# Optimization experiments

Hardware: AMD Instinct MI355X
Metric: run time of the kernel (lower is better)

Reference implementation:

```python
import jax, jax.numpy as jnp
import numpy as np

N_NODES = 100000
N_EDGES = 1600000
NFEAT = 128
NHID = 128
NS = 64
NCLASS = 16
B = 8192


def setup_inputs() -> dict:
    key = jax.random.key(0)
    ks = jax.random.split(key, 12)
    s = jax.random.normal(ks[0], (B, NS), dtype=jnp.float32)
    x = jax.random.normal(ks[1], (N_NODES, NFEAT), dtype=jnp.float32)
    row = jax.random.randint(ks[2], (N_EDGES,), 0, N_NODES)
    col = jax.random.randint(ks[3], (N_EDGES,), 0, N_NODES)
    val = jax.random.uniform(ks[4], (N_EDGES,), dtype=jnp.float32)
    index = jax.random.randint(ks[5], (B,), 0, N_NODES)
    # learned parameters (glorot-ish scale)
    W1 = jax.random.normal(ks[6], (NFEAT, NHID), dtype=jnp.float32) / np.sqrt(NFEAT)
    b1 = jnp.zeros((NHID,), dtype=jnp.float32)
    W2 = jax.random.normal(ks[7], (NHID, NHID), dtype=jnp.float32) / np.sqrt(NHID)
    b2 = jnp.zeros((NHID,), dtype=jnp.float32)
    Wl = jax.random.normal(ks[8], (NHID + NS, NCLASS), dtype=jnp.float32) / np.sqrt(NHID + NS)
    bl = jnp.zeros((NCLASS,), dtype=jnp.float32)
    return {"s": s, "x": x, "row": row, "col": col, "val": val,
            "index": index, "W1": W1, "b1": b1, "W2": W2, "b2": b2,
            "Wl": Wl, "bl": bl}


def reference(s, x, row, col, val, index, W1, b1, W2, b2, Wl, bl):
    n = x.shape[0]

    def spmm(h):
        # adj @ h with adj in COO form: out[r] += val_e * h[c]
        return jax.ops.segment_sum(val[:, None] * h[col], row, num_segments=n)

    # dropout is identity in eval mode (training=False)
    h = jax.nn.relu(spmm(x @ W1) + b1)          # gc1 + relu
    h = spmm(h @ W2) + b2                        # gc2
    z = jnp.concatenate([h[index], s], axis=1) @ Wl + bl  # [B, nclass]
    return jax.nn.log_softmax(z, axis=1)
```

## Files before the change

kernel.cpp:

```cpp
#include <hip/hip_runtime.h>
#include <math.h>

#define N_NODES 100000
#define N_EDGES 1600000
#define NFEAT 128
#define NHID 128
#define NS 64
#define NCLASS 16
#define BB 8192

#define B1_SHIFT 11
#define NB1 49
#define SUB_SHIFT 5
#define NSUB 3125
#define CHUNKA 2048
#define HWG 256
#define BINC_CAP 2048

typedef unsigned long long ull;
typedef unsigned int uint;


__device__ __forceinline__ unsigned short f2bf(float f) {
  unsigned int u = __float_as_uint(f);
  return (unsigned short)((u + 0x7fffu + ((u >> 16) & 1u)) >> 16);
}
__device__ __forceinline__ float bflo(unsigned int u) {
  return __uint_as_float(u << 16);
}
__device__ __forceinline__ float bfhi(unsigned int u) {
  return __uint_as_float(u & 0xffff0000u);
}
__device__ __forceinline__ unsigned int packbf2(float lo, float hi) {
  return (unsigned int)f2bf(lo) | ((unsigned int)f2bf(hi) << 16);
}


__device__ __forceinline__ ull pack_edge(float v, int r, int c) {
  return ((ull)(__float_as_uint(v) >> 2) << 34) | ((ull)(unsigned)r << 17) | (unsigned)c;
}
__device__ __forceinline__ int edge_col(ull p) { return (int)(p & 0x1FFFFu); }
__device__ __forceinline__ int edge_row(ull p) { return (int)((unsigned)(p >> 17) & 0x1FFFFu); }
__device__ __forceinline__ float edge_val(ull p) {
  return __uint_as_float(((unsigned)(p >> 34)) << 2);
}
__device__ __forceinline__ int keep_test(const uint* keep, int r) {
  return (keep[r >> 5] >> (r & 31)) & 1u;
}


__global__ __launch_bounds__(256) void selbuild_kernel(const int* __restrict__ index,
                                                       int* __restrict__ sel,
                                                       uint* __restrict__ keep) {
  int t = blockIdx.x * 256 + threadIdx.x;
  int r = index[t];
  sel[r] = 1;
  atomicOr(&keep[r >> 5], 1u << (r & 31));
}

__global__ __launch_bounds__(256) void selflag_kernel(const int* __restrict__ row,
                                                      const int* __restrict__ col,
                                                      const int* __restrict__ sel,
                                                      uint* __restrict__ keep) {
  int i = blockIdx.x * blockDim.x + threadIdx.x;
  int stride = gridDim.x * blockDim.x;
  for (; i < N_EDGES; i += stride)
    if (sel[row[i]]) {
      int c = col[i];
      atomicOr(&keep[c >> 5], 1u << (c & 31));
    }
}


__global__ __launch_bounds__(256) void histsub_kernel(const int* __restrict__ row,
                                                      const uint* __restrict__ keep,
                                                      int* __restrict__ subcnt) {
  __shared__ int lh[NSUB];
  int tid = threadIdx.x;
  for (int i = tid; i < NSUB; i += 256) lh[i] = 0;
  __syncthreads();
  for (long i = (long)blockIdx.x * 256 + tid; i < N_EDGES; i += (long)HWG * 256) {
    int r = row[i];
    if (keep_test(keep, r)) atomicAdd(&lh[r >> SUB_SHIFT], 1);
  }
  __syncthreads();
  for (int i = tid; i < NSUB; i += 256) {
    int c = lh[i];
    if (c) atomicAdd(&subcnt[i], c);
  }
}


__global__ __launch_bounds__(1024) void scanall_kernel(const int* __restrict__ subcnt,
                                                       int* __restrict__ sub_offs,
                                                       int* __restrict__ gcur1,
                                                       int* __restrict__ gcur2) {
  __shared__ int sd[1024];
  int tid = threadIdx.x;
  int b0 = tid * 4;
  int vv[4];
  int loc = 0;
#pragma unroll
  for (int k = 0; k < 4; ++k) {
    int i = b0 + k;
    vv[k] = (i < NSUB) ? subcnt[i] : 0;
    loc += vv[k];
  }
  sd[tid] = loc;
  __syncthreads();
  for (int o = 1; o < 1024; o <<= 1) {
    int add = (tid >= o) ? sd[tid - o] : 0;
    __syncthreads();
    sd[tid] += add;
    __syncthreads();
  }
  int pre = sd[tid] - loc;
#pragma unroll
  for (int k = 0; k < 4; ++k) {
    int i = b0 + k;
    if (i < NSUB) {
      sub_offs[i] = pre;
      gcur2[i] = pre;
      if ((i & 63) == 0) gcur1[i >> 6] = pre;
      pre += vv[k];
    }
  }
  if (tid == 1023) sub_offs[NSUB] = sd[1023];
}


__global__ __launch_bounds__(256) void binA_kernel(const int* __restrict__ row,
                                                   const int* __restrict__ col,
                                                   const float* __restrict__ val,
                                                   const uint* __restrict__ keep,
                                                   int* __restrict__ gcur1,
                                                   ull* __restrict__ ebuf1) {
  __shared__ ull stage[CHUNKA];
  __shared__ short bkt[CHUNKA];
  __shared__ int hist[NB1], lofs[NB1 + 1], lcur[NB1], gbase[NB1];
  int tid = threadIdx.x;
  for (long base = (long)blockIdx.x * CHUNKA; base < N_EDGES; base += (long)gridDim.x * CHUNKA) {
    int cnt = (int)min((long)CHUNKA, (long)N_EDGES - base);
    if (tid < NB1) hist[tid] = 0;
    __syncthreads();
    ull e[8]; int bk[8];
#pragma unroll
    for (int v = 0; v < 8; ++v) {
      int i = v * 256 + tid;
      bk[v] = -1;
      if (i < cnt) {
        long g = base + i;
        int r = row[g];
        if (keep_test(keep, r)) {
          e[v] = pack_edge(val[g], r, col[g]);
          bk[v] = r >> B1_SHIFT;
          atomicAdd(&hist[bk[v]], 1);
        }
      }
    }
    __syncthreads();
    if (tid < 64) {
      int h = (tid < NB1) ? hist[tid] : 0;
      int x = h;
      for (int o = 1; o < 64; o <<= 1) {
        int y = __shfl_up(x, o);
        if (tid >= o) x += y;
      }
      if (tid < NB1) { lofs[tid] = x - h; lcur[tid] = x - h; }
      if (tid == 63) lofs[NB1] = x;
    }
    __syncthreads();
#pragma unroll
    for (int v = 0; v < 8; ++v) {
      if (bk[v] >= 0) {
        int pos = atomicAdd(&lcur[bk[v]], 1);
        stage[pos] = e[v];
        bkt[pos] = (short)bk[v];
      }
    }
    __syncthreads();
    if (tid < NB1) {
      int h = hist[tid];
      if (h > 0) gbase[tid] = atomicAdd(&gcur1[tid], h);
    }
    __syncthreads();
    int tot = lofs[NB1];
    for (int s = tid; s < tot; s += 256) {
      int lo = bkt[s];
      ebuf1[gbase[lo] + (s - lofs[lo])] = stage[s];
    }
    __syncthreads();
  }
}


__global__ __launch_bounds__(256) void binB_kernel(const ull* __restrict__ ebuf1,
                                                   const int* __restrict__ sub_offs,
                                                   int* __restrict__ gcur2,
                                                   ull* __restrict__ edat) {
  __shared__ ull stage[CHUNKA];
  __shared__ short bkt[CHUNKA];
  __shared__ int hist[64], lofs[65], lcur[64], gbase[64];
  int tid = threadIdx.x;
  int b1 = blockIdx.x >> 3, w = blockIdx.x & 7;
  int rbeg = sub_offs[b1 << 6];
  int rend = sub_offs[min((b1 + 1) << 6, NSUB)];
  for (int base = rbeg + w * CHUNKA; base < rend; base += 8 * CHUNKA) {
    int cnt = min(CHUNKA, rend - base);
    if (tid < 64) hist[tid] = 0;
    __syncthreads();
    ull e[8]; int bk[8];
#pragma unroll
    for (int v = 0; v < 8; ++v) {
      int i = v * 256 + tid;
      bk[v] = -1;
      if (i < cnt) {
        e[v] = ebuf1[base + i];
        bk[v] = (edge_row(e[v]) >> SUB_SHIFT) - (b1 << 6);
        atomicAdd(&hist[bk[v]], 1);
      }
    }
    __syncthreads();
    if (tid < 64) {
      int h = hist[tid];
      int x = h;
      for (int o = 1; o < 64; o <<= 1) {
        int y = __shfl_up(x, o);
        if (tid >= o) x += y;
      }
      lofs[tid] = x - h;
      lcur[tid] = x - h;
      if (tid == 63) lofs[64] = x;
    }
    __syncthreads();
#pragma unroll
    for (int v = 0; v < 8; ++v) {
      if (bk[v] >= 0) {
        int pos = atomicAdd(&lcur[bk[v]], 1);
        stage[pos] = e[v];
        bkt[pos] = (short)bk[v];
      }
    }
    __syncthreads();
    if (tid < 64) {
      int h = hist[tid];
      if (h > 0) gbase[tid] = atomicAdd(&gcur2[(b1 << 6) + tid], h);
    }
    __syncthreads();
    for (int s = tid; s < cnt; s += 256) {
      int lo = bkt[s];
      edat[gbase[lo] + (s - lofs[lo])] = stage[s];
    }
    __syncthreads();
  }
}


__global__ __launch_bounds__(256) void binC_kernel(const int* __restrict__ sub_offs,
                                                   ull* __restrict__ edat,
                                                   ull* __restrict__ ebuf1,
                                                   int* __restrict__ offs) {
  __shared__ ull es[BINC_CAP];
  __shared__ int rcnt[32], rcur[32];
  int s = blockIdx.x, tid = threadIdx.x;
  int r0 = s << SUB_SHIFT;
  int beg = sub_offs[s], end = sub_offs[s + 1];
  int n = end - beg;
  if (tid < 32) rcnt[tid] = 0;
  __syncthreads();
  if (n <= BINC_CAP) {
    for (int i = tid; i < n; i += 256) {
      ull p = edat[beg + i];
      es[i] = p;
      atomicAdd(&rcnt[edge_row(p) & 31], 1);
    }
    __syncthreads();
    if (tid < 32) {
      int h = rcnt[tid];
      int x = h;
      for (int o = 1; o < 32; o <<= 1) {
        int y = __shfl_up(x, o, 32);
        if (tid >= o) x += y;
      }
      rcur[tid] = x - h;
      offs[r0 + tid] = beg + x - h;
      if (s == NSUB - 1 && tid == 31) offs[N_NODES] = end;
    }
    __syncthreads();
    for (int i = tid; i < n; i += 256) {
      ull p = es[i];
      int pos = atomicAdd(&rcur[edge_row(p) & 31], 1);
      edat[beg + pos] = p;
    }
  } else {
    for (int i = tid; i < n; i += 256) {
      ull p = edat[beg + i];
      ebuf1[beg + i] = p;
      atomicAdd(&rcnt[edge_row(p) & 31], 1);
    }
    __syncthreads();
    if (tid < 32) {
      int h = rcnt[tid];
      int x = h;
      for (int o = 1; o < 32; o <<= 1) {
        int y = __shfl_up(x, o, 32);
        if (tid >= o) x += y;
      }
      rcur[tid] = x - h;
      offs[r0 + tid] = beg + x - h;
      if (s == NSUB - 1 && tid == 31) offs[N_NODES] = end;
    }
    __syncthreads();
    for (int i = tid; i < n; i += 256) {
      ull p = ebuf1[beg + i];
      int pos = atomicAdd(&rcur[edge_row(p) & 31], 1);
      edat[beg + pos] = p;
    }
  }
}


typedef __attribute__((ext_vector_type(8))) __bf16 bf16x8;
typedef __attribute__((ext_vector_type(4))) float f32x4;
union FragU { uint4 u; bf16x8 b; };

#define LDSTR 68

__global__ __launch_bounds__(256) void gemm1_kernel(const float* __restrict__ A,
                                                    const float* __restrict__ W,
                                                    unsigned short* __restrict__ C,
                                                    int nrows) {
  __shared__ uint As_s[64 * LDSTR];
  __shared__ uint Wt_s[128 * LDSTR];
  int tid = threadIdx.x;
  int rbase = blockIdx.x * 64;

  {
    int n = tid & 127, hh = tid >> 7;
#pragma unroll
    for (int kk = 0; kk < 32; ++kk) {
      int kc = hh * 32 + kk;
      Wt_s[n * LDSTR + kc] = packbf2(W[(2 * kc) * 128 + n], W[(2 * kc + 1) * 128 + n]);
    }
  }
  {
    const float4* src = (const float4*)(A + (long)rbase * 128);
#pragma unroll
    for (int i = 0; i < 8; ++i) {
      int f = i * 256 + tid;
      int m = f >> 5;
      float4 v = (rbase + m < nrows) ? src[f] : make_float4(0.f, 0.f, 0.f, 0.f);
      int c = (f & 31) * 2;
      As_s[m * LDSTR + c]     = packbf2(v.x, v.y);
      As_s[m * LDSTR + c + 1] = packbf2(v.z, v.w);
    }
  }
  __syncthreads();

  int w = tid >> 6, lane = tid & 63;
  int quad = lane >> 4, lr = lane & 15;
  int n0 = w * 32;

  f32x4 acc[4][2];
#pragma unroll
  for (int mt = 0; mt < 4; ++mt)
#pragma unroll
    for (int nt = 0; nt < 2; ++nt) acc[mt][nt] = (f32x4){0.f, 0.f, 0.f, 0.f};

#pragma unroll
  for (int kk = 0; kk < 4; ++kk) {
    int kc = kk * 16 + quad * 4;
    FragU fb0, fb1;
    fb0.u = *(const uint4*)&Wt_s[(n0 + lr) * LDSTR + kc];
    fb1.u = *(const uint4*)&Wt_s[(n0 + 16 + lr) * LDSTR + kc];
#pragma unroll
    for (int mt = 0; mt < 4; ++mt) {
      FragU fa;
      fa.u = *(const uint4*)&As_s[(mt * 16 + lr) * LDSTR + kc];
      acc[mt][0] = __builtin_amdgcn_mfma_f32_16x16x32_bf16(fa.b, fb0.b, acc[mt][0], 0, 0, 0);
      acc[mt][1] = __builtin_amdgcn_mfma_f32_16x16x32_bf16(fa.b, fb1.b, acc[mt][1], 0, 0, 0);
    }
  }

#pragma unroll
  for (int mt = 0; mt < 4; ++mt) {
#pragma unroll
    for (int nt = 0; nt < 2; ++nt) {
      int col = n0 + nt * 16 + lr;
#pragma unroll
      for (int r = 0; r < 4; ++r) {
        int row = rbase + mt * 16 + quad * 4 + r;
        if (row < nrows) C[(long)row * 128 + col] = f2bf(acc[mt][nt][r]);
      }
    }
  }
}


__global__ __launch_bounds__(256) void gemm2f_kernel(const float* __restrict__ g2,
                                                     const float* __restrict__ W2,
                                                     const float* __restrict__ b2,
                                                     const float* __restrict__ s_in,
                                                     const float* __restrict__ Wl,
                                                     const float* __restrict__ bl,
                                                     float* __restrict__ out) {
  __shared__ uint smem[13056];
  uint* Wt_s = smem;
  uint* As_s = smem + 128 * LDSTR;
  float* ts  = (float*)smem;
  float* Wls = (float*)(smem + 128 * LDSTR);
  int tid = threadIdx.x;
  int rbase = blockIdx.x * 64;

  {
    int n = tid & 127, hh = tid >> 7;
#pragma unroll
    for (int kk = 0; kk < 32; ++kk) {
      int kc = hh * 32 + kk;
      Wt_s[n * LDSTR + kc] = packbf2(W2[(2 * kc) * 128 + n], W2[(2 * kc + 1) * 128 + n]);
    }
  }
  {
    const float4* src = (const float4*)(g2 + (long)rbase * 128);
#pragma unroll
    for (int i = 0; i < 8; ++i) {
      int f = i * 256 + tid;
      int m = f >> 5, c = (f & 31) * 2;
      float4 v = src[f];
      As_s[m * LDSTR + c]     = packbf2(v.x, v.y);
      As_s[m * LDSTR + c + 1] = packbf2(v.z, v.w);
    }
  }
  __syncthreads();

  int w = tid >> 6, lane = tid & 63;
  int quad = lane >> 4, lr = lane & 15;
  int n0 = w * 32;

  f32x4 acc[4][2];
#pragma unroll
  for (int mt = 0; mt < 4; ++mt)
#pragma unroll
    for (int nt = 0; nt < 2; ++nt) acc[mt][nt] = (f32x4){0.f, 0.f, 0.f, 0.f};

#pragma unroll
  for (int kk = 0; kk < 4; ++kk) {
    int kc = kk * 16 + quad * 4;
    FragU fb0, fb1;
    fb0.u = *(const uint4*)&Wt_s[(n0 + lr) * LDSTR + kc];
    fb1.u = *(const uint4*)&Wt_s[(n0 + 16 + lr) * LDSTR + kc];
#pragma unroll
    for (int mt = 0; mt < 4; ++mt) {
      FragU fa;
      fa.u = *(const uint4*)&As_s[(mt * 16 + lr) * LDSTR + kc];
      acc[mt][0] = __builtin_amdgcn_mfma_f32_16x16x32_bf16(fa.b, fb0.b, acc[mt][0], 0, 0, 0);
      acc[mt][1] = __builtin_amdgcn_mfma_f32_16x16x32_bf16(fa.b, fb1.b, acc[mt][1], 0, 0, 0);
    }
  }
  __syncthreads();

#pragma unroll
  for (int mt = 0; mt < 4; ++mt) {
#pragma unroll
    for (int nt = 0; nt < 2; ++nt) {
      int col = n0 + nt * 16 + lr;
      float bv = b2[col];
#pragma unroll
      for (int r = 0; r < 4; ++r)
        ts[(mt * 16 + quad * 4 + r) * 129 + col] = acc[mt][nt][r] + bv;
    }
  }
  for (int i = tid; i < 192 * 16; i += 256) Wls[i] = Wl[i];
  __syncthreads();

  int q = lane & 3;
  int mrow = w * 16 + (lane >> 2);
  int b = rbase + mrow;
  float z[16];
#pragma unroll
  for (int c = 0; c < 16; ++c) z[c] = 0.f;
  int k0 = q * 48;
  for (int kk = 0; kk < 48; ++kk) {
    int k = k0 + kk;
    float xv = (k < 128) ? ts[mrow * 129 + k] : s_in[(long)b * 64 + (k - 128)];
    const float* wp = Wls + k * 16;
#pragma unroll
    for (int c = 0; c < 16; ++c) z[c] = fmaf(xv, wp[c], z[c]);
  }
#pragma unroll
  for (int c = 0; c < 16; ++c) {
    z[c] += __shfl_xor(z[c], 1);
    z[c] += __shfl_xor(z[c], 2);
  }
  if (q == 0) {
#pragma unroll
    for (int c = 0; c < 16; ++c) z[c] += bl[c];
    float mx = z[0];
#pragma unroll
    for (int c = 1; c < 16; ++c) mx = fmaxf(mx, z[c]);
    float sum = 0.f;
#pragma unroll
    for (int c = 0; c < 16; ++c) sum += expf(z[c] - mx);
    float lse = mx + logf(sum);
    float4* ob = (float4*)(out + (long)b * 16);
    ob[0] = make_float4(z[0] - lse, z[1] - lse, z[2] - lse, z[3] - lse);
    ob[1] = make_float4(z[4] - lse, z[5] - lse, z[6] - lse, z[7] - lse);
    ob[2] = make_float4(z[8] - lse, z[9] - lse, z[10] - lse, z[11] - lse);
    ob[3] = make_float4(z[12] - lse, z[13] - lse, z[14] - lse, z[15] - lse);
  }
}


__device__ __forceinline__ void fma_row(float* acc, float v, uint4 u) {
  acc[0] = fmaf(v, bflo(u.x), acc[0]);
  acc[1] = fmaf(v, bfhi(u.x), acc[1]);
  acc[2] = fmaf(v, bflo(u.y), acc[2]);
  acc[3] = fmaf(v, bfhi(u.y), acc[3]);
  acc[4] = fmaf(v, bflo(u.z), acc[4]);
  acc[5] = fmaf(v, bfhi(u.z), acc[5]);
  acc[6] = fmaf(v, bflo(u.w), acc[6]);
  acc[7] = fmaf(v, bfhi(u.w), acc[7]);
}

__global__ __launch_bounds__(256) void spmm_row_kernel(const int* __restrict__ offs,
                                                       const ull* __restrict__ edat,
                                                       const unsigned short* __restrict__ a,
                                                       const float* __restrict__ bias,
                                                       unsigned short* __restrict__ h,
                                                       const uint* __restrict__ keep) {
  int wave = threadIdx.x >> 6;
  int lane = threadIdx.x & 63;
  int r = blockIdx.x * 4 + wave;
  if (!keep_test(keep, r)) return;
  int g = lane >> 4, l = lane & 15;
  int s = offs[r], e = offs[r + 1];
  float acc[8] = {0.f, 0.f, 0.f, 0.f, 0.f, 0.f, 0.f, 0.f};
  int j = s + g;
  for (; j + 4 < e; j += 8) {
    ull p0 = edat[j];
    ull p1 = edat[j + 4];
    uint4 u0 = *(const uint4*)(a + (long)edge_col(p0) * 128 + l * 8);
    uint4 u1 = *(const uint4*)(a + (long)edge_col(p1) * 128 + l * 8);
    fma_row(acc, edge_val(p0), u0);
    fma_row(acc, edge_val(p1), u1);
  }
  if (j < e) {
    ull p = edat[j];
    uint4 u = *(const uint4*)(a + (long)edge_col(p) * 128 + l * 8);
    fma_row(acc, edge_val(p), u);
  }
#pragma unroll
  for (int k = 0; k < 8; ++k) {
    acc[k] += __shfl_xor(acc[k], 16);
    acc[k] += __shfl_xor(acc[k], 32);
  }
  if (g == 0) {
    float4 b0 = *(const float4*)(bias + l * 8);
    float4 b1 = *(const float4*)(bias + l * 8 + 4);
    uint4 o;
    o.x = packbf2(fmaxf(acc[0] + b0.x, 0.f), fmaxf(acc[1] + b0.y, 0.f));
    o.y = packbf2(fmaxf(acc[2] + b0.z, 0.f), fmaxf(acc[3] + b0.w, 0.f));
    o.z = packbf2(fmaxf(acc[4] + b1.x, 0.f), fmaxf(acc[5] + b1.y, 0.f));
    o.w = packbf2(fmaxf(acc[6] + b1.z, 0.f), fmaxf(acc[7] + b1.w, 0.f));
    *(uint4*)(h + (long)r * 128 + l * 8) = o;
  }
}

__global__ __launch_bounds__(256) void spmm_sel_kernel(const int* __restrict__ offs,
                                                       const ull* __restrict__ edat,
                                                       const unsigned short* __restrict__ h1,
                                                       const int* __restrict__ index,
                                                       float* __restrict__ g2) {
  int wave = threadIdx.x >> 6;
  int lane = threadIdx.x & 63;
  int b = blockIdx.x * 4 + wave;
  int g = lane >> 4, l = lane & 15;
  int r = index[b];
  int s = offs[r], e = offs[r + 1];
  float acc[8] = {0.f, 0.f, 0.f, 0.f, 0.f, 0.f, 0.f, 0.f};
  int j = s + g;
  for (; j + 4 < e; j += 8) {
    ull p0 = edat[j];
    ull p1 = edat[j + 4];
    uint4 u0 = *(const uint4*)(h1 + (long)edge_col(p0) * 128 + l * 8);
    uint4 u1 = *(const uint4*)(h1 + (long)edge_col(p1) * 128 + l * 8);
    fma_row(acc, edge_val(p0), u0);
    fma_row(acc, edge_val(p1), u1);
  }
  if (j < e) {
    ull p = edat[j];
    uint4 u = *(const uint4*)(h1 + (long)edge_col(p) * 128 + l * 8);
    fma_row(acc, edge_val(p), u);
  }
#pragma unroll
  for (int k = 0; k < 8; ++k) {
    acc[k] += __shfl_xor(acc[k], 16);
    acc[k] += __shfl_xor(acc[k], 32);
  }
  if (g == 0) {
    float* op = g2 + (long)b * 128 + l * 8;
    *(float4*)(op + 0) = make_float4(acc[0], acc[1], acc[2], acc[3]);
    *(float4*)(op + 4) = make_float4(acc[4], acc[5], acc[6], acc[7]);
  }
}


extern "C" void kernel_launch(void* const* d_in, const int* in_sizes, int n_in,
                              void* d_out, int out_size, void* d_ws, size_t ws_size,
                              hipStream_t stream) {
  const float* s_in  = (const float*)d_in[0];
  const float* x     = (const float*)d_in[1];
  const int*   row   = (const int*)d_in[2];
  const int*   col   = (const int*)d_in[3];
  const float* val   = (const float*)d_in[4];
  const int*   index = (const int*)d_in[5];
  const float* W1    = (const float*)d_in[6];
  const float* b1    = (const float*)d_in[7];
  const float* W2    = (const float*)d_in[8];
  const float* b2    = (const float*)d_in[9];
  const float* Wl    = (const float*)d_in[10];
  const float* bl    = (const float*)d_in[11];
  float* out = (float*)d_out;

  ull* edat  = (ull*)d_ws;
  ull* ebuf1 = edat + N_EDGES;
  unsigned short* a  = (unsigned short*)(ebuf1 + N_EDGES);
  unsigned short* h1 = a + (size_t)N_NODES * 128;
  float* g2   = (float*)(h1 + (size_t)N_NODES * 128);
  int* sel    = (int*)(g2 + (size_t)BB * 128);
  int* subcnt = sel + N_NODES;
  uint* keep  = (uint*)(subcnt + NSUB);
  int* offs   = (int*)(keep + NSUB);
  int* sub_offs = offs + (N_NODES + 1);
  int* gcur1  = sub_offs + (NSUB + 1);
  int* gcur2  = gcur1 + NB1;

  hipMemsetAsync(sel, 0, (N_NODES + 2 * NSUB) * sizeof(int), stream);

  selbuild_kernel<<<BB / 256, 256, 0, stream>>>(index, sel, keep);
  selflag_kernel<<<4096, 256, 0, stream>>>(row, col, sel, keep);
  histsub_kernel<<<HWG, 256, 0, stream>>>(row, keep, subcnt);
  scanall_kernel<<<1, 1024, 0, stream>>>(subcnt, sub_offs, gcur1, gcur2);

  binA_kernel<<<512, 256, 0, stream>>>(row, col, val, keep, gcur1, ebuf1);
  binB_kernel<<<NB1 * 8, 256, 0, stream>>>(ebuf1, sub_offs, gcur2, edat);
  binC_kernel<<<NSUB, 256, 0, stream>>>(sub_offs, edat, ebuf1, offs);

  gemm1_kernel<<<(N_NODES + 63) / 64, 256, 0, stream>>>(x, W1, a, N_NODES);
  spmm_row_kernel<<<N_NODES / 4, 256, 0, stream>>>(offs, edat, a, b1, h1, keep);
  spmm_sel_kernel<<<BB / 4, 256, 0, stream>>>(offs, edat, h1, index, g2);
  gemm2f_kernel<<<BB / 64, 256, 0, stream>>>(g2, W2, b2, s_in, Wl, bl, out);
}
```

Baseline: 295.4 us.

## Slice features into 16-wide planes and compress edges to 4-byte quantized entries

The gemm1 output and the hidden layer h1 are stored as 8 feature slices of 16 columns, and both SpMM kernels now launch one block per (row group, slice), so each block's gathers touch a much smaller table that fits better in L2. Edges are repacked in binC into 32-bit words holding a 17-bit column and a 15-bit fixed-point value, which halves the bytes read per edge. The cost is that each edge list is read once per slice, edge weights are quantized, and the 4-byte edge array aliases the ebuf1 scratch buffer that binC's overflow path still writes to.

```diff
diff --git a/kernel.cpp b/kernel.cpp
--- a/kernel.cpp
+++ b/kernel.cpp
@@ -17,6 +17,10 @@
 #define HWG 256
 #define BINC_CAP 2048
 
+#define NSLICE 8
+#define SLICEF 16
+#define VSCALE (1.0f / 32767.0f)
+
 typedef unsigned long long ull;
 typedef unsigned int uint;
 
@@ -43,6 +47,10 @@
 __device__ __forceinline__ int edge_row(ull p) { return (int)((unsigned)(p >> 17) & 0x1FFFFu); }
 __device__ __forceinline__ float edge_val(ull p) {
   return __uint_as_float(((unsigned)(p >> 34)) << 2);
+}
+__device__ __forceinline__ uint pack4(ull p) {
+  uint q = (uint)(edge_val(p) * 32767.f + 0.5f);
+  return (uint)edge_col(p) | (q << 17);
 }
 __device__ __forceinline__ int keep_test(const uint* keep, int r) {
   return (keep[r >> 5] >> (r & 31)) & 1u;
@@ -197,7 +205,7 @@
 __global__ __launch_bounds__(256) void binB_kernel(const ull* __restrict__ ebuf1,
                                                    const int* __restrict__ sub_offs,
                                                    int* __restrict__ gcur2,
-                                                   ull* __restrict__ edat) {
+                                                   ull* __restrict__ edat8) {
   __shared__ ull stage[CHUNKA];
   __shared__ short bkt[CHUNKA];
   __shared__ int hist[64], lofs[65], lcur[64], gbase[64];
@@ -249,7 +257,7 @@
     __syncthreads();
     for (int s = tid; s < cnt; s += 256) {
       int lo = bkt[s];
-      edat[gbase[lo] + (s - lofs[lo])] = stage[s];
+      edat8[gbase[lo] + (s - lofs[lo])] = stage[s];
     }
     __syncthreads();
   }
@@ -257,8 +265,9 @@
 
 
 __global__ __launch_bounds__(256) void binC_kernel(const int* __restrict__ sub_offs,
-                                                   ull* __restrict__ edat,
+                                                   const ull* __restrict__ edat8,
                                                    ull* __restrict__ ebuf1,
+                                                   uint* __restrict__ edat4,
                                                    int* __restrict__ offs) {
   __shared__ ull es[BINC_CAP];
   __shared__ int rcnt[32], rcur[32];
@@ -270,7 +279,7 @@
   __syncthreads();
   if (n <= BINC_CAP) {
     for (int i = tid; i < n; i += 256) {
-      ull p = edat[beg + i];
+      ull p = edat8[beg + i];
       es[i] = p;
       atomicAdd(&rcnt[edge_row(p) & 31], 1);
     }
@@ -290,11 +299,11 @@
     for (int i = tid; i < n; i += 256) {
       ull p = es[i];
       int pos = atomicAdd(&rcur[edge_row(p) & 31], 1);
-      edat[beg + pos] = p;
+      edat4[beg + pos] = pack4(p);
     }
   } else {
     for (int i = tid; i < n; i += 256) {
-      ull p = edat[beg + i];
+      ull p = edat8[beg + i];
       ebuf1[beg + i] = p;
       atomicAdd(&rcnt[edge_row(p) & 31], 1);
     }
@@ -314,7 +323,7 @@
     for (int i = tid; i < n; i += 256) {
       ull p = ebuf1[beg + i];
       int pos = atomicAdd(&rcur[edge_row(p) & 31], 1);
-      edat[beg + pos] = p;
+      edat4[beg + pos] = pack4(p);
     }
   }
 }
@@ -386,11 +395,11 @@
   for (int mt = 0; mt < 4; ++mt) {
 #pragma unroll
     for (int nt = 0; nt < 2; ++nt) {
-      int col = n0 + nt * 16 + lr;
+      unsigned short* cs = C + (size_t)(w * 2 + nt) * (N_NODES * SLICEF);
 #pragma unroll
       for (int r = 0; r < 4; ++r) {
         int row = rbase + mt * 16 + quad * 4 + r;
-        if (row < nrows) C[(long)row * 128 + col] = f2bf(acc[mt][nt][r]);
+        if (row < nrows) cs[(size_t)row * SLICEF + lr] = f2bf(acc[mt][nt][r]);
       }
     }
   }
@@ -523,83 +532,88 @@
 }
 
 __global__ __launch_bounds__(256) void spmm_row_kernel(const int* __restrict__ offs,
-                                                       const ull* __restrict__ edat,
+                                                       const uint* __restrict__ edat4,
                                                        const unsigned short* __restrict__ a,
                                                        const float* __restrict__ bias,
-                                                       unsigned short* __restrict__ h,
+                                                       unsigned short* __restrict__ h1,
                                                        const uint* __restrict__ keep) {
-  int wave = threadIdx.x >> 6;
-  int lane = threadIdx.x & 63;
-  int r = blockIdx.x * 4 + wave;
+  int s = blockIdx.x & 7;
+  int rblk = blockIdx.x >> 3;
+  int tid = threadIdx.x, lane = tid & 63;
+  int r = rblk * 16 + (tid >> 4);
+  int g = (lane >> 1) & 7, h = lane & 1, h8 = h * 8;
   if (!keep_test(keep, r)) return;
-  int g = lane >> 4, l = lane & 15;
-  int s = offs[r], e = offs[r + 1];
+  const unsigned short* as = a + (size_t)s * (N_NODES * SLICEF);
+  int j = offs[r] + g, jend = offs[r + 1];
   float acc[8] = {0.f, 0.f, 0.f, 0.f, 0.f, 0.f, 0.f, 0.f};
-  int j = s + g;
-  for (; j + 4 < e; j += 8) {
-    ull p0 = edat[j];
-    ull p1 = edat[j + 4];
-    uint4 u0 = *(const uint4*)(a + (long)edge_col(p0) * 128 + l * 8);
-    uint4 u1 = *(const uint4*)(a + (long)edge_col(p1) * 128 + l * 8);
-    fma_row(acc, edge_val(p0), u0);
-    fma_row(acc, edge_val(p1), u1);
-  }
-  if (j < e) {
-    ull p = edat[j];
-    uint4 u = *(const uint4*)(a + (long)edge_col(p) * 128 + l * 8);
-    fma_row(acc, edge_val(p), u);
+  for (; j + 8 < jend; j += 16) {
+    uint e0 = edat4[j];
+    uint e1 = edat4[j + 8];
+    uint4 u0 = *(const uint4*)(as + (size_t)(e0 & 0x1FFFFu) * SLICEF + h8);
+    uint4 u1 = *(const uint4*)(as + (size_t)(e1 & 0x1FFFFu) * SLICEF + h8);
+    fma_row(acc, (float)(e0 >> 17) * VSCALE, u0);
+    fma_row(acc, (float)(e1 >> 17) * VSCALE, u1);
+  }
+  if (j < jend) {
+    uint e = edat4[j];
+    uint4 u = *(const uint4*)(as + (size_t)(e & 0x1FFFFu) * SLICEF + h8);
+    fma_row(acc, (float)(e >> 17) * VSCALE, u);
   }
 #pragma unroll
   for (int k = 0; k < 8; ++k) {
-    acc[k] += __shfl_xor(acc[k], 16);
-    acc[k] += __shfl_xor(acc[k], 32);
-  }
-  if (g == 0) {
-    float4 b0 = *(const float4*)(bias + l * 8);
-    float4 b1 = *(const float4*)(bias + l * 8 + 4);
+    acc[k] += __shfl_xor(acc[k], 2);
+    acc[k] += __shfl_xor(acc[k], 4);
+    acc[k] += __shfl_xor(acc[k], 8);
+  }
+  if ((lane & 14) == 0) {
+    const float* bp = bias + s * SLICEF + h8;
+    float4 b0 = *(const float4*)bp;
+    float4 b1v = *(const float4*)(bp + 4);
     uint4 o;
     o.x = packbf2(fmaxf(acc[0] + b0.x, 0.f), fmaxf(acc[1] + b0.y, 0.f));
     o.y = packbf2(fmaxf(acc[2] + b0.z, 0.f), fmaxf(acc[3] + b0.w, 0.f));
-    o.z = packbf2(fmaxf(acc[4] + b1.x, 0.f), fmaxf(acc[5] + b1.y, 0.f));
-    o.w = packbf2(fmaxf(acc[6] + b1.z, 0.f), fmaxf(acc[7] + b1.w, 0.f));
-    *(uint4*)(h + (long)r * 128 + l * 8) = o;
+    o.z = packbf2(fmaxf(acc[4] + b1v.x, 0.f), fmaxf(acc[5] + b1v.y, 0.f));
+    o.w = packbf2(fmaxf(acc[6] + b1v.z, 0.f), fmaxf(acc[7] + b1v.w, 0.f));
+    *(uint4*)(h1 + (size_t)s * (N_NODES * SLICEF) + (size_t)r * SLICEF + h8) = o;
   }
 }
 
 __global__ __launch_bounds__(256) void spmm_sel_kernel(const int* __restrict__ offs,
-                                                       const ull* __restrict__ edat,
+                                                       const uint* __restrict__ edat4,
                                                        const unsigned short* __restrict__ h1,
                                                        const int* __restrict__ index,
                                                        float* __restrict__ g2) {
-  int wave = threadIdx.x >> 6;
-  int lane = threadIdx.x & 63;
-  int b = blockIdx.x * 4 + wave;
-  int g = lane >> 4, l = lane & 15;
+  int s = blockIdx.x & 7;
+  int bblk = blockIdx.x >> 3;
+  int tid = threadIdx.x, lane = tid & 63;
+  int b = bblk * 16 + (tid >> 4);
+  int g = (lane >> 1) & 7, h = lane & 1, h8 = h * 8;
+  const unsigned short* hs = h1 + (size_t)s * (N_NODES * SLICEF);
   int r = index[b];
-  int s = offs[r], e = offs[r + 1];
+  int j = offs[r] + g, jend = offs[r + 1];
   float acc[8] = {0.f, 0.f, 0.f, 0.f, 0.f, 0.f, 0.f, 0.f};
-  int j = s + g;
-  for (; j + 4 < e; j += 8) {
-    ull p0 = edat[j];
-    ull p1 = edat[j + 4];
-    uint4 u0 = *(const uint4*)(h1 + (long)edge_col(p0) * 128 + l * 8);
-    uint4 u1 = *(const uint4*)(h1 + (long)edge_col(p1) * 128 + l * 8);
-    fma_row(acc, edge_val(p0), u0);
-    fma_row(acc, edge_val(p1), u1);
-  }
-  if (j < e) {
-    ull p = edat[j];
-    uint4 u = *(const uint4*)(h1 + (long)edge_col(p) * 128 + l * 8);
-    fma_row(acc, edge_val(p), u);
+  for (; j + 8 < jend; j += 16) {
+    uint e0 = edat4[j];
+    uint e1 = edat4[j + 8];
+    uint4 u0 = *(const uint4*)(hs + (size_t)(e0 & 0x1FFFFu) * SLICEF + h8);
+    uint4 u1 = *(const uint4*)(hs + (size_t)(e1 & 0x1FFFFu) * SLICEF + h8);
+    fma_row(acc, (float)(e0 >> 17) * VSCALE, u0);
+    fma_row(acc, (float)(e1 >> 17) * VSCALE, u1);
+  }
+  if (j < jend) {
+    uint e = edat4[j];
+    uint4 u = *(const uint4*)(hs + (size_t)(e & 0x1FFFFu) * SLICEF + h8);
+    fma_row(acc, (float)(e >> 17) * VSCALE, u);
   }
 #pragma unroll
   for (int k = 0; k < 8; ++k) {
-    acc[k] += __shfl_xor(acc[k], 16);
-    acc[k] += __shfl_xor(acc[k], 32);
-  }
-  if (g == 0) {
-    float* op = g2 + (long)b * 128 + l * 8;
-    *(float4*)(op + 0) = make_float4(acc[0], acc[1], acc[2], acc[3]);
+    acc[k] += __shfl_xor(acc[k], 2);
+    acc[k] += __shfl_xor(acc[k], 4);
+    acc[k] += __shfl_xor(acc[k], 8);
+  }
+  if ((lane & 14) == 0) {
+    float* op = g2 + (size_t)b * 128 + s * SLICEF + h8;
+    *(float4*)op = make_float4(acc[0], acc[1], acc[2], acc[3]);
     *(float4*)(op + 4) = make_float4(acc[4], acc[5], acc[6], acc[7]);
   }
 }
@@ -622,8 +636,9 @@
   const float* bl    = (const float*)d_in[11];
   float* out = (float*)d_out;
 
-  ull* edat  = (ull*)d_ws;
-  ull* ebuf1 = edat + N_EDGES;
+  ull* edat8 = (ull*)d_ws;
+  ull* ebuf1 = edat8 + N_EDGES;
+  uint* edat4 = (uint*)ebuf1;
   unsigned short* a  = (unsigned short*)(ebuf1 + N_EDGES);
   unsigned short* h1 = a + (size_t)N_NODES * 128;
   float* g2   = (float*)(h1 + (size_t)N_NODES * 128);
@@ -643,11 +658,11 @@
   scanall_kernel<<<1, 1024, 0, stream>>>(subcnt, sub_offs, gcur1, gcur2);
 
   binA_kernel<<<512, 256, 0, stream>>>(row, col, val, keep, gcur1, ebuf1);
-  binB_kernel<<<NB1 * 8, 256, 0, stream>>>(ebuf1, sub_offs, gcur2, edat);
-  binC_kernel<<<NSUB, 256, 0, stream>>>(sub_offs, edat, ebuf1, offs);
+  binB_kernel<<<NB1 * 8, 256, 0, stream>>>(ebuf1, sub_offs, gcur2, edat8);
+  binC_kernel<<<NSUB, 256, 0, stream>>>(sub_offs, edat8, ebuf1, edat4, offs);
 
   gemm1_kernel<<<(N_NODES + 63) / 64, 256, 0, stream>>>(x, W1, a, N_NODES);
-  spmm_row_kernel<<<N_NODES / 4, 256, 0, stream>>>(offs, edat, a, b1, h1, keep);
-  spmm_sel_kernel<<<BB / 4, 256, 0, stream>>>(offs, edat, h1, index, g2);
+  spmm_row_kernel<<<(N_NODES / 16) * NSLICE, 256, 0, stream>>>(offs, edat4, a, b1, h1, keep);
+  spmm_sel_kernel<<<(BB / 16) * NSLICE, 256, 0, stream>>>(offs, edat4, h1, index, g2);
   gemm2f_kernel<<<BB / 64, 256, 0, stream>>>(g2, W2, b2, s_in, Wl, bl, out);
 }
```

After: 332.9 us. +12.7%, slower.
